# Kernel optimization log

Measured on AMD Instinct MI355X. Metric: run time of the kernel, lower is better.

The kernel has to match this reference:

```python
import jax, jax.numpy as jnp
from jax import lax
import numpy as np

B, E, D, V, NB, R = 512, 128, 8, 50000, 4, 3  # batch, embed/hidden/classes, capsule_length, num_items, num_beh, routing iters
TP, TC, TF, TK = 50, 50, 50, 200  # purchase/cart/fav/click lengths


def setup_inputs() -> dict:
    key = jax.random.key(0)
    k = jax.random.split(key, 12)
    item_emb = jax.random.normal(k[4], (V + 1, E), jnp.float32)
    item_emb = item_emb.at[0].set(0.0)  # padding_idx=0
    return {
        "purchase_seq": jax.random.randint(k[0], (B, TP), 0, V + 1),
        "cart_seq": jax.random.randint(k[1], (B, TC), 0, V + 1),
        "fav_seq": jax.random.randint(k[2], (B, TF), 0, V + 1),
        "click_seq": jax.random.randint(k[3], (B, TK), 0, V + 1),
        "item_emb": item_emb,
        "gru_Wih": 0.1 * jax.random.normal(k[5], (NB, 3 * E, E), jnp.float32),
        "gru_Whh": 0.1 * jax.random.normal(k[6], (NB, 3 * E, E), jnp.float32),
        "gru_bih": jnp.zeros((NB, 3 * E), jnp.float32),
        "gru_bhh": jnp.zeros((NB, 3 * E), jnp.float32),
        "W": 0.01 * jax.random.uniform(k[7], (E, NB, E, D), dtype=jnp.float32),
        "w_scale": jnp.ones((E,), jnp.float32),
        "bias_vec": jnp.zeros((E,), jnp.float32),
        "alpha": jnp.full((1,), float(E), jnp.float32),
        "W_coef": 0.1 * jax.random.normal(k[8], (E, E + D, D), jnp.float32),
    }


def _gru_last(x, Wih, Whh, bih, bhh):
    """Standard GRU over x: (B, T, E); returns final hidden state (B, H)."""
    H = Whh.shape[1]

    def step(h, xt):
        gi = xt @ Wih.T + bih
        gh = h @ Whh.T + bhh
        ir, iz, inn = jnp.split(gi, 3, axis=-1)
        hr, hz, hn = jnp.split(gh, 3, axis=-1)
        r = jax.nn.sigmoid(ir + hr)
        z = jax.nn.sigmoid(iz + hz)
        n = jnp.tanh(inn + r * hn)
        return (1.0 - z) * n + z * h, None

    h0 = jnp.zeros((x.shape[0], H), x.dtype)
    h, _ = lax.scan(step, h0, jnp.swapaxes(x, 0, 1))
    return h


def _forward(seqs, item_emb, gru_Wih, gru_Whh, gru_bih, gru_bhh, W, w_scale, bias_vec, alpha, W_coef):
    hs = []
    for i, s in enumerate(seqs):  # fixed small loop over num_beh=4 structurally distinct GRUs
        emb = item_emb[s] * (s != 0)[..., None].astype(item_emb.dtype)
        hs.append(_gru_last(emb, gru_Wih[i], gru_Whh[i], gru_bih[i], gru_bhh[i]))
    e = jnp.stack(hs, axis=-1)  # (B, H, NB)  == stack(dim=1).permute(0,2,1)
    u = jnp.einsum('bht,htcd->bhcd', e, W)  # (B, H, C, D)
    b = jnp.zeros(u.shape[:3] + (1,), u.dtype)
    u_det = lax.stop_gradient(u)
    E_det = lax.stop_gradient(item_emb)
    for _ in range(R - 1):  # detached routing-by-agreement iterations
        c = jax.nn.softmax(b, axis=2)
        v = lax.stop_gradient(alpha) * jnp.sum(c * u_det, axis=1)  # (B, C, D)
        v_ = jnp.linalg.norm(v, axis=-1) * lax.stop_gradient(w_scale) + lax.stop_gradient(bias_vec)  # (B, C)
        p = jax.nn.softmax(v_ @ E_det.T, axis=-1) @ E_det  # (B, E) soft vocab lookup
        p = jnp.broadcast_to(p[:, None, :], (p.shape[0], u.shape[2], p.shape[-1]))  # (B, C, E)
        coef = jnp.einsum('bcd,cdD->bcD', jnp.concatenate([p, v], axis=-1), W_coef)  # (B, C, D)
        b = b + jnp.sum(u_det * coef[:, None], axis=-1, keepdims=True)
    c = jax.nn.softmax(b, axis=2)
    v = alpha * jnp.sum(c * u, axis=1)
    v_ = jnp.linalg.norm(v, axis=-1) * w_scale + bias_vec
    return v_ @ item_emb.T  # (B, V+1)


def reference(purchase_seq, cart_seq, fav_seq, click_seq, item_emb, gru_Wih, gru_Whh, gru_bih, gru_bhh, W, w_scale, bias_vec, alpha, W_coef):
    return _forward((purchase_seq, cart_seq, fav_seq, click_seq), item_emb, gru_Wih, gru_Whh,
                    gru_bih, gru_bhh, W, w_scale, bias_vec, alpha, W_coef)
```

## Files before the change

kernel.cpp:

```cpp
#include <hip/hip_runtime.h>
#include <math.h>

typedef __attribute__((ext_vector_type(8))) short bf16x8;
typedef __attribute__((ext_vector_type(4))) float f32x4;
typedef __attribute__((ext_vector_type(2))) float f32x2;
typedef __attribute__((ext_vector_type(4))) unsigned short u16x4;
typedef __attribute__((ext_vector_type(2))) _Float16 f16x2;

static __device__ __forceinline__ short f2bf(float f) {
  unsigned u = __builtin_bit_cast(unsigned, f);
  u += 0x7fffu + ((u >> 16) & 1u);
  return (short)(u >> 16);
}
static __device__ __forceinline__ float bf2f(unsigned short s) {
  unsigned u = ((unsigned)s) << 16;
  return __builtin_bit_cast(float, u);
}
static __device__ __forceinline__ f32x4 mfma16(bf16x8 a, bf16x8 b, f32x4 c) {
  return __builtin_amdgcn_mfma_f32_16x16x32_bf16(a, b, c, 0, 0, 0);
}
static __device__ __forceinline__ bf16x8 pack8v(f32x4 a, f32x4 b) {
  bf16x8 r;
  r[0]=f2bf(a[0]); r[1]=f2bf(a[1]); r[2]=f2bf(a[2]); r[3]=f2bf(a[3]);
  r[4]=f2bf(b[0]); r[5]=f2bf(b[1]); r[6]=f2bf(b[2]); r[7]=f2bf(b[3]);
  return r;
}
static __device__ __forceinline__ float fastrcp(float x) {
  float r;
  asm("v_rcp_f32_e32 %0, %1" : "=v"(r) : "v"(x));
  return r;
}
static __device__ __forceinline__ float dot4(f32x4 a, f32x4 b) {
  return a[0]*b[0] + a[1]*b[1] + a[2]*b[2] + a[3]*b[3];
}

#define LGKM_BARRIER() do {                                   \
    asm volatile("s_waitcnt lgkmcnt(0)" ::: "memory");        \
    __builtin_amdgcn_s_barrier();                             \
    __builtin_amdgcn_sched_barrier(0);                        \
  } while (0)

__global__ __launch_bounds__(512) void gi_gemm_kernel(
    const int* __restrict__ seq0, const int* __restrict__ seq1,
    const int* __restrict__ seq2, const int* __restrict__ seq3,
    const float* __restrict__ item_emb, const float* __restrict__ Wih,
    unsigned short* __restrict__ gi_t50, unsigned short* __restrict__ gi_click)
{
  const int b = blockIdx.x;
  int beh, tile0;
  if (b < 100)      { beh = 0; tile0 = b * 16; }
  else if (b < 200) { beh = 1; tile0 = (b - 100) * 16; }
  else if (b < 300) { beh = 2; tile0 = (b - 200) * 16; }
  else              { beh = 3; tile0 = (b - 300) * 16; }
  const int T = (beh == 3) ? 200 : 50;
  const int* seq = (beh == 0) ? seq0 : (beh == 1) ? seq1 : (beh == 2) ? seq2 : seq3;
  unsigned short* gibase = (beh == 3) ? gi_click : (gi_t50 + (size_t)beh * 9830400);

  const int tid = threadIdx.x;
  const int wave = tid >> 6, lane = tid & 63, lrow = lane & 15, lk8 = lane >> 4;
  const int bcol = wave * 16 + lrow;

  bf16x8 wif[3][4];
  const float* WihB = Wih + (size_t)beh * 384 * 128;
#pragma unroll
  for (int g = 0; g < 3; ++g) {
    const int wr = g * 128 + bcol;
#pragma unroll
    for (int kt = 0; kt < 4; ++kt) {
      const int k0 = kt * 32 + lk8 * 8;
      f32x4 a0 = *(const f32x4*)(WihB + (size_t)wr * 128 + k0);
      f32x4 a1 = *(const f32x4*)(WihB + (size_t)wr * 128 + k0 + 4);
      wif[g][kt] = pack8v(a0, a1);
    }
  }

  __shared__ short xt[16][132];
  const int gj = tid >> 5;
  const int gc = (tid & 31) * 4;

  for (int ti = 0; ti < 16; ++ti) {
    const int tile = tile0 + ti;
    const int r0blk = tile / T;
    const int t = tile - r0blk * T;
    {
      const int sidx = seq[(size_t)(r0blk * 16 + gj) * T + t];
      const f32x4 xv = *(const f32x4*)(item_emb + (size_t)sidx * 128 + gc);
      xt[gj][gc]     = f2bf(xv[0]);
      xt[gj][gc + 1] = f2bf(xv[1]);
      xt[gj][gc + 2] = f2bf(xv[2]);
      xt[gj][gc + 3] = f2bf(xv[3]);
    }
    __syncthreads();
    bf16x8 ax[4];
#pragma unroll
    for (int kt = 0; kt < 4; ++kt)
      ax[kt] = *(const bf16x8*)&xt[lrow][kt * 32 + lk8 * 8];
    f32x4 acc[3] = {{0,0,0,0},{0,0,0,0},{0,0,0,0}};
#pragma unroll
    for (int kt = 0; kt < 4; ++kt) {
      acc[0] = mfma16(ax[kt], wif[0][kt], acc[0]);
      acc[1] = mfma16(ax[kt], wif[1][kt], acc[1]);
      acc[2] = mfma16(ax[kt], wif[2][kt], acc[2]);
    }
    unsigned short* base = gibase + ((size_t)(r0blk * 4 + lk8) * T + t) * 1536;
    unsigned short* dst = base + bcol * 4;
#pragma unroll
    for (int g = 0; g < 3; ++g) {
      u16x4 o;
      o[0] = (unsigned short)f2bf(acc[g][0]);
      o[1] = (unsigned short)f2bf(acc[g][1]);
      o[2] = (unsigned short)f2bf(acc[g][2]);
      o[3] = (unsigned short)f2bf(acc[g][3]);
      *(u16x4*)(dst + g * 512) = o;
    }
    __syncthreads();
  }
}

__global__ __launch_bounds__(256, 2) void gru_rec5w_kernel(
    const float* __restrict__ Whh, const float* __restrict__ bih,
    const float* __restrict__ bhh,
    const unsigned short* __restrict__ gi_t50,
    const unsigned short* __restrict__ gi_click,
    const float* __restrict__ item_emb, unsigned short* __restrict__ Ebf,
    float* __restrict__ e_out)
{
  __shared__ short h0[16][140];
  __shared__ short h1[16][140];
  const int tid = threadIdx.x;

  if (blockIdx.x >= 512) {
    const int wb = blockIdx.x - 512;
    for (size_t i8 = (size_t)(wb * 256 + tid) * 8; i8 < 50048u * 128u; i8 += 32768u * 8u) {
      const int row = (int)(i8 >> 7);
      bf16x8 o = {0,0,0,0,0,0,0,0};
      if (row < 50001) {
        const f32x4 a = *(const f32x4*)(item_emb + i8);
        const f32x4 b = *(const f32x4*)(item_emb + i8 + 4);
        o = pack8v(a, b);
      }
      *(bf16x8*)(Ebf + i8) = o;
    }
    return;
  }

  const int beh = blockIdx.x >> 7;
  const int qt = blockIdx.x & 127;
  const int T = (beh == 3) ? 200 : 50;
  const unsigned short* gib =
      ((beh == 3) ? gi_click : (gi_t50 + (size_t)beh * 9830400)) + (size_t)qt * T * 1536;

  const int w = tid >> 6;
  const int lane = tid & 63;
  const int lrow = lane & 15;
  const int lk8 = lane >> 4;
  const int col0 = w * 32 + lrow;
  const int col1 = col0 + 16;

  bf16x8 whf[3][2][4];
  const float* WhhB = Whh + (size_t)beh * 384 * 128;
#pragma unroll
  for (int g = 0; g < 3; ++g) {
#pragma unroll
    for (int ct = 0; ct < 2; ++ct) {
      const int wr = g * 128 + (ct ? col1 : col0);
#pragma unroll
      for (int kt = 0; kt < 4; ++kt) {
        const int k0 = kt * 32 + lk8 * 8;
        f32x4 b0 = *(const f32x4*)(WhhB + (size_t)wr * 128 + k0);
        f32x4 b1 = *(const f32x4*)(WhhB + (size_t)wr * 128 + k0 + 4);
        whf[g][ct][kt] = pack8v(b0, b1);
      }
    }
  }
  float bR[2], bZ[2], bN[2], bHN[2];
#pragma unroll
  for (int ct = 0; ct < 2; ++ct) {
    const int c = ct ? col1 : col0;
    bR[ct]  = bih[beh * 384 + c] + bhh[beh * 384 + c];
    bZ[ct]  = bih[beh * 384 + 128 + c] + bhh[beh * 384 + 128 + c];
    bN[ct]  = bih[beh * 384 + 256 + c];
    bHN[ct] = bhh[beh * 384 + 256 + c];
  }

  for (int i = tid; i < 16 * 140; i += 256) { ((short*)h0)[i] = 0; ((short*)h1)[i] = 0; }
  float hreg[2] = {0.f, 0.f};
  __syncthreads();

  const unsigned short* gp0 = gib + col0 * 4 + lk8;
  const unsigned short* gp1 = gib + col1 * 4 + lk8;

  unsigned short ga[30], gb[30];

#define LOAD_CHUNK(BUF, C0) do {                                              \
    _Pragma("unroll")                                                         \
    for (int _s = 0; _s < 5; ++_s) {                                          \
      const size_t _o = (size_t)((C0) + _s) * 1536;                           \
      _Pragma("unroll")                                                       \
      for (int _g = 0; _g < 3; ++_g) {                                        \
        BUF[_s * 6 + 0 * 3 + _g] = gp0[_o + _g * 512];                        \
        BUF[_s * 6 + 1 * 3 + _g] = gp1[_o + _g * 512];                        \
      }                                                                       \
    }                                                                         \
  } while (0)

  short (*hin)[140] = h0;
  short (*hout)[140] = h1;

#define STEP(BUF, S) do {                                                     \
    bf16x8 ah[4];                                                             \
    _Pragma("unroll")                                                         \
    for (int kt = 0; kt < 4; ++kt)                                            \
      ah[kt] = *(const bf16x8*)&hin[lrow][kt * 32 + lk8 * 8];                 \
    f32x4 hr_[2], hz_[2], hn_[2];                                             \
    _Pragma("unroll")                                                         \
    for (int ct = 0; ct < 2; ++ct) {                                          \
      hr_[ct] = (f32x4){0,0,0,0}; hz_[ct] = (f32x4){0,0,0,0}; hn_[ct] = (f32x4){0,0,0,0}; \
      _Pragma("unroll")                                                       \
      for (int kt = 0; kt < 4; ++kt) {                                        \
        hr_[ct] = mfma16(ah[kt], whf[0][ct][kt], hr_[ct]);                    \
        hz_[ct] = mfma16(ah[kt], whf[1][ct][kt], hz_[ct]);                    \
        hn_[ct] = mfma16(ah[kt], whf[2][ct][kt], hn_[ct]);                    \
      }                                                                       \
    }                                                                         \
    _Pragma("unroll")                                                         \
    for (int ct = 0; ct < 2; ++ct) {                                          \
      const float xr = bf2f(BUF[(S)*6 + ct*3 + 0]) + bR[ct] + hr_[ct][0];     \
      const float xz = bf2f(BUF[(S)*6 + ct*3 + 1]) + bZ[ct] + hz_[ct][0];     \
      const float ea = __expf(-xr);                                           \
      const float eb = __expf(-xz);                                           \
      const float pa = 1.f + ea, pb = 1.f + eb;                               \
      const float rd = fastrcp(pa * pb);                                      \
      const float rr = pb * rd;                                               \
      const float zz = pa * rd;                                               \
      const float tn = bf2f(BUF[(S)*6 + ct*3 + 2]) + bN[ct] + rr * (hn_[ct][0] + bHN[ct]); \
      const float tt = __expf(-2.f * tn);                                     \
      const float nn = (1.f - tt) * fastrcp(1.f + tt);                        \
      hreg[ct] = nn + zz * (hreg[ct] - nn);                                   \
      hout[lk8 * 4][ct ? col1 : col0] = f2bf(hreg[ct]);                       \
    }                                                                         \
    LGKM_BARRIER();                                                           \
    short (*_tmp)[140] = hin; hin = hout; hout = _tmp;                        \
  } while (0)

  LOAD_CHUNK(ga, 0);
  for (int c = 0; c < T; c += 10) {
    if (c + 5 < T) LOAD_CHUNK(gb, c + 5);
    STEP(ga, 0); STEP(ga, 1); STEP(ga, 2); STEP(ga, 3); STEP(ga, 4);
    if (c + 10 < T) LOAD_CHUNK(ga, c + 10);
    STEP(gb, 0); STEP(gb, 1); STEP(gb, 2); STEP(gb, 3); STEP(gb, 4);
  }
#undef STEP
#undef LOAD_CHUNK

#pragma unroll
  for (int ct = 0; ct < 2; ++ct)
    e_out[(size_t)(qt * 4 + lk8) * 512 + (ct ? col1 : col0) * 4 + beh] = hreg[ct];
}

template<int MODE>
__global__ __launch_bounds__(256, 1) void route_kernel(
    const _Float16* __restrict__ b_old, _Float16* __restrict__ b_new,
    const float* __restrict__ e_buf, const float* __restrict__ W,
    const float* __restrict__ coef_buf,
    const float* __restrict__ w_scale, const float* __restrict__ bias_vec,
    const float* __restrict__ alpha,
    float* __restrict__ v_buf, float* __restrict__ vn_buf)
{
  __shared__ float e_lds[4][128][4];
  __shared__ float vacc[4][4][128][8];
  const int g0 = blockIdx.x * 4;
  const int tid = threadIdx.x;
  const int wv = tid >> 6, ln = tid & 63;
  const int c0 = ln * 2;
  for (int i = tid; i < 2048; i += 256) ((float*)e_lds)[i] = e_buf[(size_t)g0 * 512 + i];

  f32x4 cf[4][2][2];
  if (MODE != 0) {
#pragma unroll
    for (int g = 0; g < 4; ++g)
#pragma unroll
      for (int cc = 0; cc < 2; ++cc) {
        cf[g][cc][0] = *(const f32x4*)(coef_buf + (size_t)(g0 + g) * 1024 + (c0 + cc) * 8);
        cf[g][cc][1] = *(const f32x4*)(coef_buf + (size_t)(g0 + g) * 1024 + (c0 + cc) * 8 + 4);
      }
  }
  __syncthreads();

  f32x4 av[4][2][2];
#pragma unroll
  for (int g = 0; g < 4; ++g)
#pragma unroll
    for (int cc = 0; cc < 2; ++cc) { av[g][cc][0] = (f32x4){0,0,0,0}; av[g][cc][1] = (f32x4){0,0,0,0}; }

  const int hbeg = wv * 32;
  for (int h = hbeg; h < hbeg + 32; ++h) {
    f32x4 wr[4][2][2];
#pragma unroll
    for (int t = 0; t < 4; ++t) {
      const float* wp = W + ((size_t)(h * 4 + t) * 128 + c0) * 8;
      wr[t][0][0] = *(const f32x4*)(wp);
      wr[t][0][1] = *(const f32x4*)(wp + 4);
      wr[t][1][0] = *(const f32x4*)(wp + 8);
      wr[t][1][1] = *(const f32x4*)(wp + 12);
    }
    f16x2 bo[4];
    if (MODE == 2) {
#pragma unroll
      for (int g = 0; g < 4; ++g)
        bo[g] = *(const f16x2*)(b_old + (size_t)(g0 + g) * 16384 + h * 128 + c0);
    }
#pragma unroll
    for (int g = 0; g < 4; ++g) {
      const f32x4 ev = *(const f32x4*)&e_lds[g][h][0];
      f32x4 u[2][2];
#pragma unroll
      for (int cc = 0; cc < 2; ++cc)
#pragma unroll
        for (int dd = 0; dd < 2; ++dd)
          u[cc][dd] = ev[0]*wr[0][cc][dd] + ev[1]*wr[1][cc][dd]
                    + ev[2]*wr[2][cc][dd] + ev[3]*wr[3][cc][dd];
      float cv0, cv1;
      if (MODE == 0) {
        cv0 = 0.0078125f; cv1 = 0.0078125f;
      } else {
        float b0 = dot4(u[0][0], cf[g][0][0]) + dot4(u[0][1], cf[g][0][1]);
        float b1 = dot4(u[1][0], cf[g][1][0]) + dot4(u[1][1], cf[g][1][1]);
        if (MODE == 2) { b0 += (float)bo[g][0]; b1 += (float)bo[g][1]; }
        if (MODE == 1) {
          f16x2 bw; bw[0] = (_Float16)b0; bw[1] = (_Float16)b1;
          *(f16x2*)(b_new + (size_t)(g0 + g) * 16384 + h * 128 + c0) = bw;
        }
        float m = fmaxf(b0, b1);
#pragma unroll
        for (int off = 32; off > 0; off >>= 1) m = fmaxf(m, __shfl_xor(m, off));
        const float e0 = __expf(b0 - m), e1 = __expf(b1 - m);
        float s = e0 + e1;
#pragma unroll
        for (int off = 32; off > 0; off >>= 1) s += __shfl_xor(s, off);
        const float inv = 1.f / s;
        cv0 = e0 * inv; cv1 = e1 * inv;
      }
      av[g][0][0] += cv0 * u[0][0]; av[g][0][1] += cv0 * u[0][1];
      av[g][1][0] += cv1 * u[1][0]; av[g][1][1] += cv1 * u[1][1];
    }
  }
#pragma unroll
  for (int g = 0; g < 4; ++g)
#pragma unroll
    for (int cc = 0; cc < 2; ++cc) {
      *(f32x4*)&vacc[wv][g][c0 + cc][0] = av[g][cc][0];
      *(f32x4*)&vacc[wv][g][c0 + cc][4] = av[g][cc][1];
    }
  __syncthreads();

  const float al = alpha[0];
  const int rg = tid >> 6;
  const int rc = (tid & 63) * 2;
#pragma unroll
  for (int cc = 0; cc < 2; ++cc) {
    const int c = rc + cc;
    f32x4 s0 = *(const f32x4*)&vacc[0][rg][c][0];
    f32x4 s1 = *(const f32x4*)&vacc[0][rg][c][4];
#pragma unroll
    for (int wq = 1; wq < 4; ++wq) {
      s0 += *(const f32x4*)&vacc[wq][rg][c][0];
      s1 += *(const f32x4*)&vacc[wq][rg][c][4];
    }
    s0 *= al; s1 *= al;
    *(f32x4*)(v_buf + (size_t)(g0 + rg) * 1024 + c * 8) = s0;
    *(f32x4*)(v_buf + (size_t)(g0 + rg) * 1024 + c * 8 + 4) = s1;
    const float ss = dot4(s0, s0) + dot4(s1, s1);
    vn_buf[(g0 + rg) * 128 + c] = sqrtf(ss) * w_scale[c] + bias_vec[c];
  }
}

__global__ __launch_bounds__(256, 2) void flash_kernel(
    const float* __restrict__ vn, const unsigned short* __restrict__ Ebf,
    float* __restrict__ o_part, float* __restrict__ ms_part)
{
  __shared__ short e_nat[64][136];
  __shared__ short e_tr[128][72];
  __shared__ short p_lds[4][16][72];
  const int xc = blockIdx.x;
  const int tid = threadIdx.x;
  const int w = tid >> 6, lane = tid & 63, lrow = lane & 15, lk8 = lane >> 4;
  const int rowbase = blockIdx.y * 64 + w * 16;

  bf16x8 qf[4];
#pragma unroll
  for (int kt = 0; kt < 4; ++kt) {
    const float* p = vn + (size_t)(rowbase + lrow) * 128 + kt * 32 + lk8 * 8;
    qf[kt] = pack8v(*(const f32x4*)p, *(const f32x4*)(p + 4));
  }

  f32x4 o_acc[8] = {{0,0,0,0},{0,0,0,0},{0,0,0,0},{0,0,0,0},
                    {0,0,0,0},{0,0,0,0},{0,0,0,0},{0,0,0,0}};
  float m_run[4] = {-1e30f, -1e30f, -1e30f, -1e30f};
  float s_run[4] = {0.f, 0.f, 0.f, 0.f};

  const int kbeg = xc * 1024;
  const int nst = (kbeg + 1024 <= 50048) ? 16 : (50048 - kbeg) / 64;
  const int sr = tid >> 2, sseg = (tid & 3) * 32;

  for (int st = 0; st < nst; ++st) {
    const int v0 = kbeg + st * 64;
    {
      bf16x8 ev[4];
#pragma unroll
      for (int q = 0; q < 4; ++q)
        ev[q] = *(const bf16x8*)(Ebf + (size_t)(v0 + sr) * 128 + sseg + q * 8);
#pragma unroll
      for (int q = 0; q < 4; ++q)
        *(bf16x8*)&e_nat[sr][sseg + q * 8] = ev[q];
#pragma unroll
      for (int q = 0; q < 4; ++q)
#pragma unroll
        for (int j = 0; j < 8; ++j)
          e_tr[sseg + q * 8 + j][sr] = ev[q][j];
    }
    __syncthreads();
    f32x4 sacc[4] = {{0,0,0,0},{0,0,0,0},{0,0,0,0},{0,0,0,0}};
#pragma unroll
    for (int kt = 0; kt < 4; ++kt) {
#pragma unroll
      for (int nt = 0; nt < 4; ++nt) {
        const bf16x8 bfr = *(const bf16x8*)&e_nat[nt * 16 + lrow][kt * 32 + lk8 * 8];
        sacc[nt] = mfma16(qf[kt], bfr, sacc[nt]);
      }
    }
    if (v0 + 64 > 50001) {
#pragma unroll
      for (int nt = 0; nt < 4; ++nt)
        if (v0 + nt * 16 + lrow >= 50001)
          sacc[nt] = (f32x4){-1e30f, -1e30f, -1e30f, -1e30f};
    }
#pragma unroll
    for (int e2 = 0; e2 < 4; ++e2) {
      float mt = fmaxf(fmaxf(sacc[0][e2], sacc[1][e2]), fmaxf(sacc[2][e2], sacc[3][e2]));
      mt = fmaxf(mt, __shfl_xor(mt, 1));
      mt = fmaxf(mt, __shfl_xor(mt, 2));
      mt = fmaxf(mt, __shfl_xor(mt, 4));
      mt = fmaxf(mt, __shfl_xor(mt, 8));
      const float mn = fmaxf(m_run[e2], mt);
      const float scale = __expf(m_run[e2] - mn);
      m_run[e2] = mn;
      float pv[4];
#pragma unroll
      for (int nt = 0; nt < 4; ++nt) pv[nt] = __expf(sacc[nt][e2] - mn);
      float ps = pv[0] + pv[1] + pv[2] + pv[3];
      ps += __shfl_xor(ps, 1);
      ps += __shfl_xor(ps, 2);
      ps += __shfl_xor(ps, 4);
      ps += __shfl_xor(ps, 8);
      s_run[e2] = s_run[e2] * scale + ps;
#pragma unroll
      for (int nt8 = 0; nt8 < 8; ++nt8) o_acc[nt8][e2] *= scale;
#pragma unroll
      for (int nt = 0; nt < 4; ++nt)
        p_lds[w][lk8 * 4 + e2][nt * 16 + lrow] = f2bf(pv[nt]);
    }
#pragma unroll
    for (int kt2 = 0; kt2 < 2; ++kt2) {
      const bf16x8 pa = *(const bf16x8*)&p_lds[w][lrow][kt2 * 32 + lk8 * 8];
#pragma unroll
      for (int nt8 = 0; nt8 < 8; ++nt8) {
        const bf16x8 bfr = *(const bf16x8*)&e_tr[nt8 * 16 + lrow][kt2 * 32 + lk8 * 8];
        o_acc[nt8] = mfma16(pa, bfr, o_acc[nt8]);
      }
    }
    __syncthreads();
  }

#pragma unroll
  for (int nt8 = 0; nt8 < 8; ++nt8)
#pragma unroll
    for (int e2 = 0; e2 < 4; ++e2)
      o_part[((size_t)xc * 512 + rowbase + lk8 * 4 + e2) * 128 + nt8 * 16 + lrow] = o_acc[nt8][e2];
  if (lrow == 0) {
#pragma unroll
    for (int e2 = 0; e2 < 4; ++e2) {
      const int row = rowbase + lk8 * 4 + e2;
      ms_part[((size_t)row * 49 + xc) * 2]     = m_run[e2];
      ms_part[((size_t)row * 49 + xc) * 2 + 1] = s_run[e2];
    }
  }
}

__global__ __launch_bounds__(256) void combine_coef_kernel(
    const float* __restrict__ o_part, const float* __restrict__ ms_part,
    const float* __restrict__ v_buf, const float* __restrict__ W_coef,
    float* __restrict__ coef_buf)
{
  __shared__ float wg[4][64];
  __shared__ float p_s[4][128];
  const int g0 = blockIdx.x * 4;
  const int tid = threadIdx.x;
  const int w = tid >> 6, lane = tid & 63;
  {
    const int row = g0 + w;
    float ml = -1e30f, sl = 0.f;
    if (lane < 49) {
      ml = ms_part[((size_t)row * 49 + lane) * 2];
      sl = ms_part[((size_t)row * 49 + lane) * 2 + 1];
    }
    float M = ml;
#pragma unroll
    for (int off = 32; off > 0; off >>= 1) M = fmaxf(M, __shfl_xor(M, off));
    float e = (lane < 49) ? sl * __expf(ml - M) : 0.f;
    float S = e;
#pragma unroll
    for (int off = 32; off > 0; off >>= 1) S += __shfl_xor(S, off);
    const float inv = 1.f / S;
    if (lane < 49) wg[w][lane] = __expf(ml - M) * inv;
  }
  __syncthreads();
  {
    const int d = tid & 127, gh = tid >> 7;
    for (int gg = gh; gg < 4; gg += 2) {
      const int row = g0 + gg;
      float acc = 0.f;
      for (int x = 0; x < 49; ++x)
        acc += o_part[((size_t)x * 512 + row) * 128 + d] * wg[gg][x];
      p_s[gg][d] = acc;
    }
  }
  __syncthreads();
  const int c = tid >> 1, dh = (tid & 1) * 4;
  float vg[4][8];
#pragma unroll
  for (int g = 0; g < 4; ++g) {
    const f32x4 va = *(const f32x4*)(v_buf + (size_t)(g0 + g) * 1024 + c * 8);
    const f32x4 vb = *(const f32x4*)(v_buf + (size_t)(g0 + g) * 1024 + c * 8 + 4);
    vg[g][0]=va[0]; vg[g][1]=va[1]; vg[g][2]=va[2]; vg[g][3]=va[3];
    vg[g][4]=vb[0]; vg[g][5]=vb[1]; vg[g][6]=vb[2]; vg[g][7]=vb[3];
  }
  const float* wc = W_coef + (size_t)c * 1088 + dh;
  f32x4 acc4[4] = {{0,0,0,0},{0,0,0,0},{0,0,0,0},{0,0,0,0}};
  for (int dp = 0; dp < 128; ++dp) {
    const f32x4 w4 = *(const f32x4*)(wc + (size_t)dp * 8);
#pragma unroll
    for (int g = 0; g < 4; ++g) acc4[g] += p_s[g][dp] * w4;
  }
#pragma unroll
  for (int q = 0; q < 8; ++q) {
    const f32x4 w4 = *(const f32x4*)(wc + (size_t)(128 + q) * 8);
#pragma unroll
    for (int g = 0; g < 4; ++g) acc4[g] += vg[g][q] * w4;
  }
#pragma unroll
  for (int g = 0; g < 4; ++g)
    *(f32x4*)(coef_buf + (size_t)(g0 + g) * 1024 + c * 8 + dh) = acc4[g];
}

__global__ __launch_bounds__(512) void logits32_kernel(
    const float* __restrict__ vn, const float* __restrict__ E,
    float* __restrict__ out)
{
  __shared__ short et[64][136];
  const int n0 = blockIdx.x * 64;
  const int tid = threadIdx.x;
  const int wave = tid >> 6, lane = tid & 63, lrow = lane & 15, lk8 = lane >> 4;
  {
    const int r = tid >> 3, ks = (tid & 7) * 16;
    const int v = n0 + r;
    f32x4 a = {0,0,0,0}, b = {0,0,0,0}, c = {0,0,0,0}, d = {0,0,0,0};
    if (v < 50001) {
      const float* p = E + (size_t)v * 128 + ks;
      a = *(const f32x4*)p; b = *(const f32x4*)(p + 4);
      c = *(const f32x4*)(p + 8); d = *(const f32x4*)(p + 12);
    }
    *(bf16x8*)&et[r][ks] = pack8v(a, b);
    *(bf16x8*)&et[r][ks + 8] = pack8v(c, d);
  }
  __syncthreads();
  for (int mb = 0; mb < 4; ++mb) {
    const int m0 = mb * 128;
    const int arow = m0 + wave * 16 + lrow;
    bf16x8 afr[4];
#pragma unroll
    for (int kt = 0; kt < 4; ++kt) {
      const float* p = vn + (size_t)arow * 128 + kt * 32 + lk8 * 8;
      afr[kt] = pack8v(*(const f32x4*)p, *(const f32x4*)(p + 4));
    }
    f32x4 acc[4] = {{0,0,0,0},{0,0,0,0},{0,0,0,0},{0,0,0,0}};
#pragma unroll
    for (int kt = 0; kt < 4; ++kt) {
#pragma unroll
      for (int nt = 0; nt < 4; ++nt) {
        const bf16x8 bfr = *(const bf16x8*)&et[nt * 16 + lrow][kt * 32 + lk8 * 8];
        acc[nt] = mfma16(afr[kt], bfr, acc[nt]);
      }
    }
#pragma unroll
    for (int nt = 0; nt < 4; ++nt) {
      const int col = n0 + nt * 16 + lrow;
      if (col < 50001) {
        const int row = m0 + wave * 16 + lk8 * 4;
#pragma unroll
        for (int e2 = 0; e2 < 4; ++e2)
          out[(size_t)(row + e2) * 50001 + col] = acc[nt][e2];
      }
    }
  }
}

extern "C" void kernel_launch(void* const* d_in, const int* in_sizes, int n_in,
                              void* d_out, int out_size, void* d_ws, size_t ws_size,
                              hipStream_t stream) {
  const int* seq0 = (const int*)d_in[0];
  const int* seq1 = (const int*)d_in[1];
  const int* seq2 = (const int*)d_in[2];
  const int* seq3 = (const int*)d_in[3];
  const float* item_emb = (const float*)d_in[4];
  const float* Wih = (const float*)d_in[5];
  const float* Whh = (const float*)d_in[6];
  const float* bih = (const float*)d_in[7];
  const float* bhh = (const float*)d_in[8];
  const float* W = (const float*)d_in[9];
  const float* w_scale = (const float*)d_in[10];
  const float* bias_vec = (const float*)d_in[11];
  const float* alpha = (const float*)d_in[12];
  const float* W_coef = (const float*)d_in[13];
  float* out = (float*)d_out;

  char* ws = (char*)d_ws;
  float* e_buf       = (float*)(ws);
  _Float16* b_state  = (_Float16*)(ws + 1048576);
  float* v_buf    = (float*)(ws + 34603008);
  float* vn_buf   = (float*)(ws + 36700160);
  float* coef_buf = (float*)(ws + 37224448);
  float* o_part   = (float*)(ws + 39325696);
  float* ms_part  = (float*)(ws + 52170752);

  unsigned short* gi_t50   = (unsigned short*)(ws + 1048576);
  unsigned short* gi_click = (unsigned short*)d_out;
  unsigned short* Ebf = (unsigned short*)((char*)d_out + 78643200);

  gi_gemm_kernel<<<dim3(700), 512, 0, stream>>>(seq0, seq1, seq2, seq3, item_emb, Wih,
                                                gi_t50, gi_click);
  gru_rec5w_kernel<<<dim3(640), 256, 0, stream>>>(Whh, bih, bhh, gi_t50, gi_click,
                                                  item_emb, Ebf, e_buf);
  route_kernel<0><<<dim3(128), 256, 0, stream>>>(nullptr, nullptr, e_buf, W, nullptr,
                                                 w_scale, bias_vec, alpha, v_buf, vn_buf);
  flash_kernel<<<dim3(49, 8), 256, 0, stream>>>(vn_buf, Ebf, o_part, ms_part);
  combine_coef_kernel<<<dim3(128), 256, 0, stream>>>(o_part, ms_part, v_buf, W_coef, coef_buf);
  route_kernel<1><<<dim3(128), 256, 0, stream>>>(nullptr, b_state, e_buf, W, coef_buf,
                                                 w_scale, bias_vec, alpha, v_buf, vn_buf);
  flash_kernel<<<dim3(49, 8), 256, 0, stream>>>(vn_buf, Ebf, o_part, ms_part);
  combine_coef_kernel<<<dim3(128), 256, 0, stream>>>(o_part, ms_part, v_buf, W_coef, coef_buf);
  route_kernel<2><<<dim3(128), 256, 0, stream>>>(b_state, nullptr, e_buf, W, coef_buf,
                                                 w_scale, bias_vec, alpha, v_buf, vn_buf);
  logits32_kernel<<<dim3(782), 512, 0, stream>>>(vn_buf, item_emb, out);
}
```

Before: 659.0 us.

## Split GRU recurrence to one batch row per block across more workgroups

The GRU recurrence kernel now gives each block a single batch row instead of four, raising the grid from 512 recurrence blocks to 2048. Click-sequence blocks (T=200) are scheduled first. Only lanes with lk8==0 load the gate inputs, compute the gates and write h. This shortens the per-block serial chain's dependence on a shared 16-row tile and spreads the work over more CUs, but it wastes three quarters of each MFMA tile and reloads Whh once per row. The h LDS rows 1-15 stay zero, so the results are still correct.

```diff
diff --git a/kernel.cpp b/kernel.cpp
--- a/kernel.cpp
+++ b/kernel.cpp
@@ -117,7 +117,7 @@
   }
 }
 
-__global__ __launch_bounds__(256, 2) void gru_rec5w_kernel(
+__global__ __launch_bounds__(256, 2) void gru_rec6_kernel(
     const float* __restrict__ Whh, const float* __restrict__ bih,
     const float* __restrict__ bhh,
     const unsigned short* __restrict__ gi_t50,
@@ -129,8 +129,8 @@
   __shared__ short h1[16][140];
   const int tid = threadIdx.x;
 
-  if (blockIdx.x >= 512) {
-    const int wb = blockIdx.x - 512;
+  if (blockIdx.x >= 2048) {
+    const int wb = blockIdx.x - 2048;
     for (size_t i8 = (size_t)(wb * 256 + tid) * 8; i8 < 50048u * 128u; i8 += 32768u * 8u) {
       const int row = (int)(i8 >> 7);
       bf16x8 o = {0,0,0,0,0,0,0,0};
@@ -144,11 +144,13 @@
     return;
   }
 
-  const int beh = blockIdx.x >> 7;
-  const int qt = blockIdx.x & 127;
+  int beh, row;
+  if (blockIdx.x < 512) { beh = 3; row = blockIdx.x; }
+  else { beh = (blockIdx.x - 512) >> 9; row = (blockIdx.x - 512) & 511; }
   const int T = (beh == 3) ? 200 : 50;
+  const int quad = row >> 2, rq = row & 3;
   const unsigned short* gib =
-      ((beh == 3) ? gi_click : (gi_t50 + (size_t)beh * 9830400)) + (size_t)qt * T * 1536;
+      ((beh == 3) ? gi_click : (gi_t50 + (size_t)beh * 9830400)) + (size_t)quad * T * 1536;
 
   const int w = tid >> 6;
   const int lane = tid & 63;
@@ -187,19 +189,23 @@
   float hreg[2] = {0.f, 0.f};
   __syncthreads();
 
-  const unsigned short* gp0 = gib + col0 * 4 + lk8;
-  const unsigned short* gp1 = gib + col1 * 4 + lk8;
-
-  unsigned short ga[30], gb[30];
+  const unsigned short* gp0 = gib + col0 * 4 + rq;
+  const unsigned short* gp1 = gib + col1 * 4 + rq;
+
+  unsigned short ga[10], gb[10];
+
+  unsigned short gA[30], gB[30];
 
 #define LOAD_CHUNK(BUF, C0) do {                                              \
-    _Pragma("unroll")                                                         \
-    for (int _s = 0; _s < 5; ++_s) {                                          \
-      const size_t _o = (size_t)((C0) + _s) * 1536;                           \
+    if (lk8 == 0) {                                                           \
       _Pragma("unroll")                                                       \
-      for (int _g = 0; _g < 3; ++_g) {                                        \
-        BUF[_s * 6 + 0 * 3 + _g] = gp0[_o + _g * 512];                        \
-        BUF[_s * 6 + 1 * 3 + _g] = gp1[_o + _g * 512];                        \
+      for (int _s = 0; _s < 5; ++_s) {                                        \
+        const size_t _o = (size_t)((C0) + _s) * 1536;                         \
+        _Pragma("unroll")                                                     \
+        for (int _g = 0; _g < 3; ++_g) {                                      \
+          BUF[_s * 6 + 0 * 3 + _g] = gp0[_o + _g * 512];                      \
+          BUF[_s * 6 + 1 * 3 + _g] = gp1[_o + _g * 512];                      \
+        }                                                                     \
       }                                                                       \
     }                                                                         \
   } while (0)
@@ -223,39 +229,43 @@
         hn_[ct] = mfma16(ah[kt], whf[2][ct][kt], hn_[ct]);                    \
       }                                                                       \
     }                                                                         \
-    _Pragma("unroll")                                                         \
-    for (int ct = 0; ct < 2; ++ct) {                                          \
-      const float xr = bf2f(BUF[(S)*6 + ct*3 + 0]) + bR[ct] + hr_[ct][0];     \
-      const float xz = bf2f(BUF[(S)*6 + ct*3 + 1]) + bZ[ct] + hz_[ct][0];     \
-      const float ea = __expf(-xr);                                           \
-      const float eb = __expf(-xz);                                           \
-      const float pa = 1.f + ea, pb = 1.f + eb;                               \
-      const float rd = fastrcp(pa * pb);                                      \
-      const float rr = pb * rd;                                               \
-      const float zz = pa * rd;                                               \
-      const float tn = bf2f(BUF[(S)*6 + ct*3 + 2]) + bN[ct] + rr * (hn_[ct][0] + bHN[ct]); \
-      const float tt = __expf(-2.f * tn);                                     \
-      const float nn = (1.f - tt) * fastrcp(1.f + tt);                        \
-      hreg[ct] = nn + zz * (hreg[ct] - nn);                                   \
-      hout[lk8 * 4][ct ? col1 : col0] = f2bf(hreg[ct]);                       \
+    if (lk8 == 0) {                                                           \
+      _Pragma("unroll")                                                       \
+      for (int ct = 0; ct < 2; ++ct) {                                        \
+        const float xr = bf2f(BUF[(S)*6 + ct*3 + 0]) + bR[ct] + hr_[ct][0];   \
+        const float xz = bf2f(BUF[(S)*6 + ct*3 + 1]) + bZ[ct] + hz_[ct][0];   \
+        const float ea = __expf(-xr);                                         \
+        const float eb = __expf(-xz);                                         \
+        const float pa = 1.f + ea, pb = 1.f + eb;                             \
+        const float rd = fastrcp(pa * pb);                                    \
+        const float rr = pb * rd;                                             \
+        const float zz = pa * rd;                                             \
+        const float tn = bf2f(BUF[(S)*6 + ct*3 + 2]) + bN[ct] + rr * (hn_[ct][0] + bHN[ct]); \
+        const float tt = __expf(-2.f * tn);                                   \
+        const float nn = (1.f - tt) * fastrcp(1.f + tt);                      \
+        hreg[ct] = nn + zz * (hreg[ct] - nn);                                 \
+        hout[0][ct ? col1 : col0] = f2bf(hreg[ct]);                           \
+      }                                                                       \
     }                                                                         \
     LGKM_BARRIER();                                                           \
     short (*_tmp)[140] = hin; hin = hout; hout = _tmp;                        \
   } while (0)
 
-  LOAD_CHUNK(ga, 0);
+  LOAD_CHUNK(gA, 0);
   for (int c = 0; c < T; c += 10) {
-    if (c + 5 < T) LOAD_CHUNK(gb, c + 5);
-    STEP(ga, 0); STEP(ga, 1); STEP(ga, 2); STEP(ga, 3); STEP(ga, 4);
-    if (c + 10 < T) LOAD_CHUNK(ga, c + 10);
-    STEP(gb, 0); STEP(gb, 1); STEP(gb, 2); STEP(gb, 3); STEP(gb, 4);
+    if (c + 5 < T) LOAD_CHUNK(gB, c + 5);
+    STEP(gA, 0); STEP(gA, 1); STEP(gA, 2); STEP(gA, 3); STEP(gA, 4);
+    if (c + 10 < T) LOAD_CHUNK(gA, c + 10);
+    STEP(gB, 0); STEP(gB, 1); STEP(gB, 2); STEP(gB, 3); STEP(gB, 4);
   }
 #undef STEP
 #undef LOAD_CHUNK
 
-#pragma unroll
-  for (int ct = 0; ct < 2; ++ct)
-    e_out[(size_t)(qt * 4 + lk8) * 512 + (ct ? col1 : col0) * 4 + beh] = hreg[ct];
+  if (lk8 == 0) {
+#pragma unroll
+    for (int ct = 0; ct < 2; ++ct)
+      e_out[(size_t)row * 512 + (ct ? col1 : col0) * 4 + beh] = hreg[ct];
+  }
 }
 
 template<int MODE>
@@ -639,7 +649,7 @@
 
   gi_gemm_kernel<<<dim3(700), 512, 0, stream>>>(seq0, seq1, seq2, seq3, item_emb, Wih,
                                                 gi_t50, gi_click);
-  gru_rec5w_kernel<<<dim3(640), 256, 0, stream>>>(Whh, bih, bhh, gi_t50, gi_click,
+  gru_rec6_kernel<<<dim3(2176), 256, 0, stream>>>(Whh, bih, bhh, gi_t50, gi_click,
                                                   item_emb, Ebf, e_buf);
   route_kernel<0><<<dim3(128), 256, 0, stream>>>(nullptr, nullptr, e_buf, W, nullptr,
                                                  w_scale, bias_vec, alpha, v_buf, vn_buf);
```

After: 892.0 us. 1.35x slower.

## Process two independent batch tiles per GRU recurrence block to interleave MFMA chains

Applied to the files above, without the earlier changes.

Each recurrence block now carries two independent 16-row batch tiles (A and B) through the GRU time loop, interleaving their MFMA chains and gate epilogues so the latency of one dependent step chain is hidden by the other. This halves the number of recurrence blocks, puts the long click sequences in the lowest block indices so they start first, and drops launch bounds to one block per SIMD group to allow more registers. The cost is double register pressure for the gate buffers and accumulators, and fewer concurrent blocks on the device, which may lower occupancy-based latency hiding.

```diff
diff --git a/kernel.cpp b/kernel.cpp
--- a/kernel.cpp
+++ b/kernel.cpp
@@ -117,7 +117,7 @@
   }
 }
 
-__global__ __launch_bounds__(256, 2) void gru_rec5w_kernel(
+__global__ __launch_bounds__(256, 1) void gru_rec7_kernel(
     const float* __restrict__ Whh, const float* __restrict__ bih,
     const float* __restrict__ bhh,
     const unsigned short* __restrict__ gi_t50,
@@ -125,12 +125,14 @@
     const float* __restrict__ item_emb, unsigned short* __restrict__ Ebf,
     float* __restrict__ e_out)
 {
-  __shared__ short h0[16][140];
-  __shared__ short h1[16][140];
+  __shared__ short hA0[16][140];
+  __shared__ short hA1[16][140];
+  __shared__ short hB0[16][140];
+  __shared__ short hB1[16][140];
   const int tid = threadIdx.x;
 
-  if (blockIdx.x >= 512) {
-    const int wb = blockIdx.x - 512;
+  if (blockIdx.x >= 256) {
+    const int wb = blockIdx.x - 256;
     for (size_t i8 = (size_t)(wb * 256 + tid) * 8; i8 < 50048u * 128u; i8 += 32768u * 8u) {
       const int row = (int)(i8 >> 7);
       bf16x8 o = {0,0,0,0,0,0,0,0};
@@ -144,11 +146,15 @@
     return;
   }
 
-  const int beh = blockIdx.x >> 7;
-  const int qt = blockIdx.x & 127;
+  int beh, pr;
+  if (blockIdx.x < 64) { beh = 3; pr = blockIdx.x; }
+  else { beh = (blockIdx.x - 64) >> 6; pr = (blockIdx.x - 64) & 63; }
   const int T = (beh == 3) ? 200 : 50;
-  const unsigned short* gib =
-      ((beh == 3) ? gi_click : (gi_t50 + (size_t)beh * 9830400)) + (size_t)qt * T * 1536;
+  const int qA = pr * 2, qB = pr * 2 + 1;
+  const unsigned short* gibase =
+      (beh == 3) ? gi_click : (gi_t50 + (size_t)beh * 9830400);
+  const unsigned short* gibA = gibase + (size_t)qA * T * 1536;
+  const unsigned short* gibB = gibase + (size_t)qB * T * 1536;
 
   const int w = tid >> 6;
   const int lane = tid & 63;
@@ -183,79 +189,106 @@
     bHN[ct] = bhh[beh * 384 + 256 + c];
   }
 
-  for (int i = tid; i < 16 * 140; i += 256) { ((short*)h0)[i] = 0; ((short*)h1)[i] = 0; }
-  float hreg[2] = {0.f, 0.f};
+  for (int i = tid; i < 16 * 140; i += 256) {
+    ((short*)hA0)[i] = 0; ((short*)hA1)[i] = 0;
+    ((short*)hB0)[i] = 0; ((short*)hB1)[i] = 0;
+  }
+  float hregA[2] = {0.f, 0.f}, hregB[2] = {0.f, 0.f};
   __syncthreads();
 
-  const unsigned short* gp0 = gib + col0 * 4 + lk8;
-  const unsigned short* gp1 = gib + col1 * 4 + lk8;
-
-  unsigned short ga[30], gb[30];
-
-#define LOAD_CHUNK(BUF, C0) do {                                              \
+  const unsigned short* gpA0 = gibA + col0 * 4 + lk8;
+  const unsigned short* gpA1 = gibA + col1 * 4 + lk8;
+  const unsigned short* gpB0 = gibB + col0 * 4 + lk8;
+  const unsigned short* gpB1 = gibB + col1 * 4 + lk8;
+
+  unsigned short cAa[30], cAb[30], cBa[30], cBb[30];
+
+#define LOAD_CHUNK2(BA, BB, C0) do {                                          \
     _Pragma("unroll")                                                         \
     for (int _s = 0; _s < 5; ++_s) {                                          \
       const size_t _o = (size_t)((C0) + _s) * 1536;                           \
       _Pragma("unroll")                                                       \
       for (int _g = 0; _g < 3; ++_g) {                                        \
-        BUF[_s * 6 + 0 * 3 + _g] = gp0[_o + _g * 512];                        \
-        BUF[_s * 6 + 1 * 3 + _g] = gp1[_o + _g * 512];                        \
+        BA[_s * 6 + 0 * 3 + _g] = gpA0[_o + _g * 512];                        \
+        BA[_s * 6 + 1 * 3 + _g] = gpA1[_o + _g * 512];                        \
+        BB[_s * 6 + 0 * 3 + _g] = gpB0[_o + _g * 512];                        \
+        BB[_s * 6 + 1 * 3 + _g] = gpB1[_o + _g * 512];                        \
       }                                                                       \
     }                                                                         \
   } while (0)
 
-  short (*hin)[140] = h0;
-  short (*hout)[140] = h1;
-
-#define STEP(BUF, S) do {                                                     \
-    bf16x8 ah[4];                                                             \
+  short (*hinA)[140] = hA0;
+  short (*houtA)[140] = hA1;
+  short (*hinB)[140] = hB0;
+  short (*houtB)[140] = hB1;
+
+#define EPI(BUF, S, ct, hr_, hn_, hz_, hreg_, hout_) do {                     \
+    const float xr = bf2f(BUF[(S)*6 + (ct)*3 + 0]) + bR[ct] + hr_[ct][0];     \
+    const float xz = bf2f(BUF[(S)*6 + (ct)*3 + 1]) + bZ[ct] + hz_[ct][0];     \
+    const float ea = __expf(-xr);                                             \
+    const float eb = __expf(-xz);                                             \
+    const float pa = 1.f + ea, pb = 1.f + eb;                                 \
+    const float rd = fastrcp(pa * pb);                                        \
+    const float rr = pb * rd;                                                 \
+    const float zz = pa * rd;                                                 \
+    const float tn = bf2f(BUF[(S)*6 + (ct)*3 + 2]) + bN[ct] + rr * (hn_[ct][0] + bHN[ct]); \
+    const float tt = __expf(-2.f * tn);                                       \
+    const float nn = (1.f - tt) * fastrcp(1.f + tt);                          \
+    hreg_[ct] = nn + zz * (hreg_[ct] - nn);                                   \
+    hout_[lk8 * 4][(ct) ? col1 : col0] = f2bf(hreg_[ct]);                     \
+  } while (0)
+
+#define STEP2(BA, BB, S) do {                                                 \
+    bf16x8 ahA[4], ahB[4];                                                    \
     _Pragma("unroll")                                                         \
-    for (int kt = 0; kt < 4; ++kt)                                            \
-      ah[kt] = *(const bf16x8*)&hin[lrow][kt * 32 + lk8 * 8];                 \
-    f32x4 hr_[2], hz_[2], hn_[2];                                             \
+    for (int kt = 0; kt < 4; ++kt) {                                          \
+      ahA[kt] = *(const bf16x8*)&hinA[lrow][kt * 32 + lk8 * 8];               \
+      ahB[kt] = *(const bf16x8*)&hinB[lrow][kt * 32 + lk8 * 8];               \
+    }                                                                         \
+    f32x4 hrA[2], hzA[2], hnA[2], hrB[2], hzB[2], hnB[2];                     \
     _Pragma("unroll")                                                         \
     for (int ct = 0; ct < 2; ++ct) {                                          \
-      hr_[ct] = (f32x4){0,0,0,0}; hz_[ct] = (f32x4){0,0,0,0}; hn_[ct] = (f32x4){0,0,0,0}; \
+      hrA[ct] = (f32x4){0,0,0,0}; hzA[ct] = (f32x4){0,0,0,0}; hnA[ct] = (f32x4){0,0,0,0}; \
+      hrB[ct] = (f32x4){0,0,0,0}; hzB[ct] = (f32x4){0,0,0,0}; hnB[ct] = (f32x4){0,0,0,0}; \
       _Pragma("unroll")                                                       \
       for (int kt = 0; kt < 4; ++kt) {                                        \
-        hr_[ct] = mfma16(ah[kt], whf[0][ct][kt], hr_[ct]);                    \
-        hz_[ct] = mfma16(ah[kt], whf[1][ct][kt], hz_[ct]);                    \
-        hn_[ct] = mfma16(ah[kt], whf[2][ct][kt], hn_[ct]);                    \
+        hrA[ct] = mfma16(ahA[kt], whf[0][ct][kt], hrA[ct]);                   \
+        hrB[ct] = mfma16(ahB[kt], whf[0][ct][kt], hrB[ct]);                   \
+        hzA[ct] = mfma16(ahA[kt], whf[1][ct][kt], hzA[ct]);                   \
+        hzB[ct] = mfma16(ahB[kt], whf[1][ct][kt], hzB[ct]);                   \
+        hnA[ct] = mfma16(ahA[kt], whf[2][ct][kt], hnA[ct]);                   \
+        hnB[ct] = mfma16(ahB[kt], whf[2][ct][kt], hnB[ct]);                   \
       }                                                                       \
     }                                                                         \
     _Pragma("unroll")                                                         \
     for (int ct = 0; ct < 2; ++ct) {                                          \
-      const float xr = bf2f(BUF[(S)*6 + ct*3 + 0]) + bR[ct] + hr_[ct][0];     \
-      const float xz = bf2f(BUF[(S)*6 + ct*3 + 1]) + bZ[ct] + hz_[ct][0];     \
-      const float ea = __expf(-xr);                                           \
-      const float eb = __expf(-xz);                                           \
-      const float pa = 1.f + ea, pb = 1.f + eb;                               \
-      const float rd = fastrcp(pa * pb);                                      \
-      const float rr = pb * rd;                                               \
-      const float zz = pa * rd;                                               \
-      const float tn = bf2f(BUF[(S)*6 + ct*3 + 2]) + bN[ct] + rr * (hn_[ct][0] + bHN[ct]); \
-      const float tt = __expf(-2.f * tn);                                     \
-      const float nn = (1.f - tt) * fastrcp(1.f + tt);                        \
-      hreg[ct] = nn + zz * (hreg[ct] - nn);                                   \
-      hout[lk8 * 4][ct ? col1 : col0] = f2bf(hreg[ct]);                       \
+      EPI(BA, S, ct, hrA, hnA, hzA, hregA, houtA);                            \
+      EPI(BB, S, ct, hrB, hnB, hzB, hregB, houtB);                            \
     }                                                                         \
     LGKM_BARRIER();                                                           \
-    short (*_tmp)[140] = hin; hin = hout; hout = _tmp;                        \
+    short (*_t)[140];                                                         \
+    _t = hinA; hinA = houtA; houtA = _t;                                      \
+    _t = hinB; hinB = houtB; houtB = _t;                                      \
   } while (0)
 
-  LOAD_CHUNK(ga, 0);
+  LOAD_CHUNK2(cAa, cBa, 0);
   for (int c = 0; c < T; c += 10) {
-    if (c + 5 < T) LOAD_CHUNK(gb, c + 5);
-    STEP(ga, 0); STEP(ga, 1); STEP(ga, 2); STEP(ga, 3); STEP(ga, 4);
-    if (c + 10 < T) LOAD_CHUNK(ga, c + 10);
-    STEP(gb, 0); STEP(gb, 1); STEP(gb, 2); STEP(gb, 3); STEP(gb, 4);
-  }
-#undef STEP
-#undef LOAD_CHUNK
-
-#pragma unroll
-  for (int ct = 0; ct < 2; ++ct)
-    e_out[(size_t)(qt * 4 + lk8) * 512 + (ct ? col1 : col0) * 4 + beh] = hreg[ct];
+    if (c + 5 < T) LOAD_CHUNK2(cAb, cBb, c + 5);
+    STEP2(cAa, cBa, 0); STEP2(cAa, cBa, 1); STEP2(cAa, cBa, 2);
+    STEP2(cAa, cBa, 3); STEP2(cAa, cBa, 4);
+    if (c + 10 < T) LOAD_CHUNK2(cAa, cBa, c + 10);
+    STEP2(cAb, cBb, 0); STEP2(cAb, cBb, 1); STEP2(cAb, cBb, 2);
+    STEP2(cAb, cBb, 3); STEP2(cAb, cBb, 4);
+  }
+#undef STEP2
+#undef EPI
+#undef LOAD_CHUNK2
+
+#pragma unroll
+  for (int ct = 0; ct < 2; ++ct) {
+    e_out[(size_t)(qA * 4 + lk8) * 512 + (ct ? col1 : col0) * 4 + beh] = hregA[ct];
+    e_out[(size_t)(qB * 4 + lk8) * 512 + (ct ? col1 : col0) * 4 + beh] = hregB[ct];
+  }
 }
 
 template<int MODE>
@@ -639,8 +672,8 @@
 
   gi_gemm_kernel<<<dim3(700), 512, 0, stream>>>(seq0, seq1, seq2, seq3, item_emb, Wih,
                                                 gi_t50, gi_click);
-  gru_rec5w_kernel<<<dim3(640), 256, 0, stream>>>(Whh, bih, bhh, gi_t50, gi_click,
-                                                  item_emb, Ebf, e_buf);
+  gru_rec7_kernel<<<dim3(384), 256, 0, stream>>>(Whh, bih, bhh, gi_t50, gi_click,
+                                                 item_emb, Ebf, e_buf);
   route_kernel<0><<<dim3(128), 256, 0, stream>>>(nullptr, nullptr, e_buf, W, nullptr,
                                                  w_scale, bias_vec, alpha, v_buf, vn_buf);
   flash_kernel<<<dim3(49, 8), 256, 0, stream>>>(vn_buf, Ebf, o_part, ms_part);
```

Result: slower. 798.6 us, median of 2 (+21.2%).

## Fuse combine_coef into route kernel and prefetch embedding gather in gi GEMM

Applied to the files above, without the earlier changes.

Moves the softmax-combine of flash partials and the W_coef projection into the routing kernel, keeping the coefficients in shared memory instead of a global coef buffer and removing two kernel launches. Separately, the input-gate GEMM now prefetches the next tile's sequence index and embedding row before computing the current tile, hiding gather latency. The fusion increases LDS use per routing block and serialises the coefficient computation ahead of routing work within the same 128 blocks.

```diff
diff --git a/kernel.cpp b/kernel.cpp
--- a/kernel.cpp
+++ b/kernel.cpp
@@ -78,19 +78,30 @@
   const int gj = tid >> 5;
   const int gc = (tid & 31) * 4;
 
+#define SEQ_ADDR(TI, OUT) do {                                    \
+    const int _tile = tile0 + (TI);                               \
+    const int _r0 = _tile / T;                                    \
+    const int _t = _tile - _r0 * T;                               \
+    OUT = seq[(size_t)(_r0 * 16 + gj) * T + _t];                  \
+  } while (0)
+
+  int sidx_cur, sidx_nxt = 0;
+  SEQ_ADDR(0, sidx_cur);
+  f32x4 xv_cur = *(const f32x4*)(item_emb + (size_t)sidx_cur * 128 + gc);
+  SEQ_ADDR(1, sidx_nxt);
+
   for (int ti = 0; ti < 16; ++ti) {
-    const int tile = tile0 + ti;
-    const int r0blk = tile / T;
-    const int t = tile - r0blk * T;
-    {
-      const int sidx = seq[(size_t)(r0blk * 16 + gj) * T + t];
-      const f32x4 xv = *(const f32x4*)(item_emb + (size_t)sidx * 128 + gc);
-      xt[gj][gc]     = f2bf(xv[0]);
-      xt[gj][gc + 1] = f2bf(xv[1]);
-      xt[gj][gc + 2] = f2bf(xv[2]);
-      xt[gj][gc + 3] = f2bf(xv[3]);
-    }
+    xt[gj][gc]     = f2bf(xv_cur[0]);
+    xt[gj][gc + 1] = f2bf(xv_cur[1]);
+    xt[gj][gc + 2] = f2bf(xv_cur[2]);
+    xt[gj][gc + 3] = f2bf(xv_cur[3]);
     __syncthreads();
+    f32x4 xv_nxt = {0.f, 0.f, 0.f, 0.f};
+    int sidx_n2 = 0;
+    if (ti + 1 < 16)
+      xv_nxt = *(const f32x4*)(item_emb + (size_t)sidx_nxt * 128 + gc);
+    if (ti + 2 < 16) SEQ_ADDR(ti + 2, sidx_n2);
+
     bf16x8 ax[4];
 #pragma unroll
     for (int kt = 0; kt < 4; ++kt)
@@ -102,19 +113,27 @@
       acc[1] = mfma16(ax[kt], wif[1][kt], acc[1]);
       acc[2] = mfma16(ax[kt], wif[2][kt], acc[2]);
     }
-    unsigned short* base = gibase + ((size_t)(r0blk * 4 + lk8) * T + t) * 1536;
-    unsigned short* dst = base + bcol * 4;
-#pragma unroll
-    for (int g = 0; g < 3; ++g) {
-      u16x4 o;
-      o[0] = (unsigned short)f2bf(acc[g][0]);
-      o[1] = (unsigned short)f2bf(acc[g][1]);
-      o[2] = (unsigned short)f2bf(acc[g][2]);
-      o[3] = (unsigned short)f2bf(acc[g][3]);
-      *(u16x4*)(dst + g * 512) = o;
+    {
+      const int tile = tile0 + ti;
+      const int r0blk = tile / T;
+      const int t = tile - r0blk * T;
+      unsigned short* base = gibase + ((size_t)(r0blk * 4 + lk8) * T + t) * 1536;
+      unsigned short* dst = base + bcol * 4;
+#pragma unroll
+      for (int g = 0; g < 3; ++g) {
+        u16x4 o;
+        o[0] = (unsigned short)f2bf(acc[g][0]);
+        o[1] = (unsigned short)f2bf(acc[g][1]);
+        o[2] = (unsigned short)f2bf(acc[g][2]);
+        o[3] = (unsigned short)f2bf(acc[g][3]);
+        *(u16x4*)(dst + g * 512) = o;
+      }
     }
     __syncthreads();
-  }
+    xv_cur = xv_nxt;
+    sidx_nxt = sidx_n2;
+  }
+#undef SEQ_ADDR
 }
 
 __global__ __launch_bounds__(256, 2) void gru_rec5w_kernel(
@@ -262,30 +281,93 @@
 __global__ __launch_bounds__(256, 1) void route_kernel(
     const _Float16* __restrict__ b_old, _Float16* __restrict__ b_new,
     const float* __restrict__ e_buf, const float* __restrict__ W,
-    const float* __restrict__ coef_buf,
+    const float* __restrict__ o_part, const float* __restrict__ ms_part,
+    const float* __restrict__ W_coef,
     const float* __restrict__ w_scale, const float* __restrict__ bias_vec,
     const float* __restrict__ alpha,
     float* __restrict__ v_buf, float* __restrict__ vn_buf)
 {
   __shared__ float e_lds[4][128][4];
   __shared__ float vacc[4][4][128][8];
+  __shared__ float cf_lds[4][128][8];
+  __shared__ float wg[4][64];
+  __shared__ float p_s[4][128];
   const int g0 = blockIdx.x * 4;
   const int tid = threadIdx.x;
   const int wv = tid >> 6, ln = tid & 63;
   const int c0 = ln * 2;
   for (int i = tid; i < 2048; i += 256) ((float*)e_lds)[i] = e_buf[(size_t)g0 * 512 + i];
 
+  if (MODE != 0) {
+    {
+      const int row = g0 + wv;
+      float ml = -1e30f, sl = 0.f;
+      if (ln < 49) {
+        ml = ms_part[((size_t)row * 49 + ln) * 2];
+        sl = ms_part[((size_t)row * 49 + ln) * 2 + 1];
+      }
+      float M = ml;
+#pragma unroll
+      for (int off = 32; off > 0; off >>= 1) M = fmaxf(M, __shfl_xor(M, off));
+      float e = (ln < 49) ? sl * __expf(ml - M) : 0.f;
+      float S = e;
+#pragma unroll
+      for (int off = 32; off > 0; off >>= 1) S += __shfl_xor(S, off);
+      const float inv = 1.f / S;
+      if (ln < 49) wg[wv][ln] = __expf(ml - M) * inv;
+    }
+    __syncthreads();
+    {
+      const int d = tid & 127, gh = tid >> 7;
+      for (int gg = gh; gg < 4; gg += 2) {
+        const int row = g0 + gg;
+        float acc = 0.f;
+        for (int x = 0; x < 49; ++x)
+          acc += o_part[((size_t)x * 512 + row) * 128 + d] * wg[gg][x];
+        p_s[gg][d] = acc;
+      }
+    }
+    __syncthreads();
+    {
+      const int c = tid >> 1, dh = (tid & 1) * 4;
+      float vg[4][8];
+#pragma unroll
+      for (int g = 0; g < 4; ++g) {
+        const f32x4 va = *(const f32x4*)(v_buf + (size_t)(g0 + g) * 1024 + c * 8);
+        const f32x4 vb = *(const f32x4*)(v_buf + (size_t)(g0 + g) * 1024 + c * 8 + 4);
+        vg[g][0]=va[0]; vg[g][1]=va[1]; vg[g][2]=va[2]; vg[g][3]=va[3];
+        vg[g][4]=vb[0]; vg[g][5]=vb[1]; vg[g][6]=vb[2]; vg[g][7]=vb[3];
+      }
+      const float* wc = W_coef + (size_t)c * 1088 + dh;
+      f32x4 acc4[4] = {{0,0,0,0},{0,0,0,0},{0,0,0,0},{0,0,0,0}};
+      for (int dp = 0; dp < 128; ++dp) {
+        const f32x4 w4 = *(const f32x4*)(wc + (size_t)dp * 8);
+#pragma unroll
+        for (int g = 0; g < 4; ++g) acc4[g] += p_s[g][dp] * w4;
+      }
+#pragma unroll
+      for (int q = 0; q < 8; ++q) {
+        const f32x4 w4 = *(const f32x4*)(wc + (size_t)(128 + q) * 8);
+#pragma unroll
+        for (int g = 0; g < 4; ++g) acc4[g] += vg[g][q] * w4;
+      }
+#pragma unroll
+      for (int g = 0; g < 4; ++g)
+        *(f32x4*)&cf_lds[g][c][dh] = acc4[g];
+    }
+  }
+  __syncthreads();
+
   f32x4 cf[4][2][2];
   if (MODE != 0) {
 #pragma unroll
     for (int g = 0; g < 4; ++g)
 #pragma unroll
       for (int cc = 0; cc < 2; ++cc) {
-        cf[g][cc][0] = *(const f32x4*)(coef_buf + (size_t)(g0 + g) * 1024 + (c0 + cc) * 8);
-        cf[g][cc][1] = *(const f32x4*)(coef_buf + (size_t)(g0 + g) * 1024 + (c0 + cc) * 8 + 4);
-      }
-  }
-  __syncthreads();
+        cf[g][cc][0] = *(const f32x4*)&cf_lds[g][c0 + cc][0];
+        cf[g][cc][1] = *(const f32x4*)&cf_lds[g][c0 + cc][4];
+      }
+  }
 
   f32x4 av[4][2][2];
 #pragma unroll
@@ -485,72 +567,6 @@
       ms_part[((size_t)row * 49 + xc) * 2 + 1] = s_run[e2];
     }
   }
-}
-
-__global__ __launch_bounds__(256) void combine_coef_kernel(
-    const float* __restrict__ o_part, const float* __restrict__ ms_part,
-    const float* __restrict__ v_buf, const float* __restrict__ W_coef,
-    float* __restrict__ coef_buf)
-{
-  __shared__ float wg[4][64];
-  __shared__ float p_s[4][128];
-  const int g0 = blockIdx.x * 4;
-  const int tid = threadIdx.x;
-  const int w = tid >> 6, lane = tid & 63;
-  {
-    const int row = g0 + w;
-    float ml = -1e30f, sl = 0.f;
-    if (lane < 49) {
-      ml = ms_part[((size_t)row * 49 + lane) * 2];
-      sl = ms_part[((size_t)row * 49 + lane) * 2 + 1];
-    }
-    float M = ml;
-#pragma unroll
-    for (int off = 32; off > 0; off >>= 1) M = fmaxf(M, __shfl_xor(M, off));
-    float e = (lane < 49) ? sl * __expf(ml - M) : 0.f;
-    float S = e;
-#pragma unroll
-    for (int off = 32; off > 0; off >>= 1) S += __shfl_xor(S, off);
-    const float inv = 1.f / S;
-    if (lane < 49) wg[w][lane] = __expf(ml - M) * inv;
-  }
-  __syncthreads();
-  {
-    const int d = tid & 127, gh = tid >> 7;
-    for (int gg = gh; gg < 4; gg += 2) {
-      const int row = g0 + gg;
-      float acc = 0.f;
-      for (int x = 0; x < 49; ++x)
-        acc += o_part[((size_t)x * 512 + row) * 128 + d] * wg[gg][x];
-      p_s[gg][d] = acc;
-    }
-  }
-  __syncthreads();
-  const int c = tid >> 1, dh = (tid & 1) * 4;
-  float vg[4][8];
-#pragma unroll
-  for (int g = 0; g < 4; ++g) {
-    const f32x4 va = *(const f32x4*)(v_buf + (size_t)(g0 + g) * 1024 + c * 8);
-    const f32x4 vb = *(const f32x4*)(v_buf + (size_t)(g0 + g) * 1024 + c * 8 + 4);
-    vg[g][0]=va[0]; vg[g][1]=va[1]; vg[g][2]=va[2]; vg[g][3]=va[3];
-    vg[g][4]=vb[0]; vg[g][5]=vb[1]; vg[g][6]=vb[2]; vg[g][7]=vb[3];
-  }
-  const float* wc = W_coef + (size_t)c * 1088 + dh;
-  f32x4 acc4[4] = {{0,0,0,0},{0,0,0,0},{0,0,0,0},{0,0,0,0}};
-  for (int dp = 0; dp < 128; ++dp) {
-    const f32x4 w4 = *(const f32x4*)(wc + (size_t)dp * 8);
-#pragma unroll
-    for (int g = 0; g < 4; ++g) acc4[g] += p_s[g][dp] * w4;
-  }
-#pragma unroll
-  for (int q = 0; q < 8; ++q) {
-    const f32x4 w4 = *(const f32x4*)(wc + (size_t)(128 + q) * 8);
-#pragma unroll
-    for (int g = 0; g < 4; ++g) acc4[g] += vg[g][q] * w4;
-  }
-#pragma unroll
-  for (int g = 0; g < 4; ++g)
-    *(f32x4*)(coef_buf + (size_t)(g0 + g) * 1024 + c * 8 + dh) = acc4[g];
 }
 
 __global__ __launch_bounds__(512) void logits32_kernel(
@@ -629,7 +645,6 @@
   _Float16* b_state  = (_Float16*)(ws + 1048576);
   float* v_buf    = (float*)(ws + 34603008);
   float* vn_buf   = (float*)(ws + 36700160);
-  float* coef_buf = (float*)(ws + 37224448);
   float* o_part   = (float*)(ws + 39325696);
   float* ms_part  = (float*)(ws + 52170752);
 
@@ -641,15 +656,16 @@
                                                 gi_t50, gi_click);
   gru_rec5w_kernel<<<dim3(640), 256, 0, stream>>>(Whh, bih, bhh, gi_t50, gi_click,
                                                   item_emb, Ebf, e_buf);
-  route_kernel<0><<<dim3(128), 256, 0, stream>>>(nullptr, nullptr, e_buf, W, nullptr,
+  route_kernel<0><<<dim3(128), 256, 0, stream>>>(nullptr, nullptr, e_buf, W,
+                                                 nullptr, nullptr, W_coef,
                                                  w_scale, bias_vec, alpha, v_buf, vn_buf);
   flash_kernel<<<dim3(49, 8), 256, 0, stream>>>(vn_buf, Ebf, o_part, ms_part);
-  combine_coef_kernel<<<dim3(128), 256, 0, stream>>>(o_part, ms_part, v_buf, W_coef, coef_buf);
-  route_kernel<1><<<dim3(128), 256, 0, stream>>>(nullptr, b_state, e_buf, W, coef_buf,
+  route_kernel<1><<<dim3(128), 256, 0, stream>>>(nullptr, b_state, e_buf, W,
+                                                 o_part, ms_part, W_coef,
                                                  w_scale, bias_vec, alpha, v_buf, vn_buf);
   flash_kernel<<<dim3(49, 8), 256, 0, stream>>>(vn_buf, Ebf, o_part, ms_part);
-  combine_coef_kernel<<<dim3(128), 256, 0, stream>>>(o_part, ms_part, v_buf, W_coef, coef_buf);
-  route_kernel<2><<<dim3(128), 256, 0, stream>>>(b_state, nullptr, e_buf, W, coef_buf,
+  route_kernel<2><<<dim3(128), 256, 0, stream>>>(b_state, nullptr, e_buf, W,
+                                                 o_part, ms_part, W_coef,
                                                  w_scale, bias_vec, alpha, v_buf, vn_buf);
   logits32_kernel<<<dim3(782), 512, 0, stream>>>(vn_buf, item_emb, out);
 }
```

After: 645.2 us. 2.1% less time.
